# Optimization experiments

Measured on AMD Instinct MI355X. Metric: run time of the kernel, lower is better.

The kernel has to match this reference:

```python
import jax, jax.numpy as jnp
import numpy as np

N = 50000
E = 1600000
D_IN = 512   # embedding_num - 1
D_OUT = 512  # output1_dim


def setup_inputs() -> dict:
    key = jax.random.key(0)
    ks = jax.random.split(key, 16)
    A1_tensor = jax.random.normal(ks[0], (N, D_IN + 1), dtype=jnp.float32)
    adj_rows = jax.random.randint(ks[1], (E,), 0, N, dtype=jnp.int32)
    adj_cols = jax.random.randint(ks[2], (E,), 0, N, dtype=jnp.int32)
    adj_vals = jax.random.uniform(ks[3], (E,), dtype=jnp.float32)
    s = 1.0 / np.sqrt(D_IN)
    Lin1 = jax.random.uniform(ks[4], (D_IN, D_OUT), minval=-s, maxval=s, dtype=jnp.float32)
    Lin1_bias = jax.random.uniform(ks[5], (D_OUT,), minval=-s, maxval=s, dtype=jnp.float32)
    n = jax.random.uniform(ks[6], (N, 1), minval=0.0, maxval=1.0, dtype=jnp.float32)
    W1 = jax.random.uniform(ks[7], (D_IN, D_OUT), minval=-s, maxval=s, dtype=jnp.float32)
    b1 = jax.random.uniform(ks[8], (D_OUT,), minval=-s, maxval=s, dtype=jnp.float32)
    s2 = 1.0 / np.sqrt(D_OUT)
    W2 = jax.random.uniform(ks[9], (D_OUT, D_OUT), minval=-s2, maxval=s2, dtype=jnp.float32)
    b2 = jax.random.uniform(ks[10], (D_OUT,), minval=-s2, maxval=s2, dtype=jnp.float32)
    W3 = jax.random.uniform(ks[11], (D_OUT, D_OUT), minval=-s2, maxval=s2, dtype=jnp.float32)
    b3 = jax.random.uniform(ks[12], (D_OUT,), minval=-s2, maxval=s2, dtype=jnp.float32)
    return {"A1_tensor": A1_tensor, "adj_rows": adj_rows, "adj_cols": adj_cols,
            "adj_vals": adj_vals, "Lin1": Lin1, "Lin1_bias": Lin1_bias, "n": n,
            "W1": W1, "b1": b1, "W2": W2, "b2": b2, "W3": W3, "b3": b3}


def reference(A1_tensor, adj_rows, adj_cols, adj_vals, Lin1, Lin1_bias, n,
              W1, b1, W2, b2, W3, b3):
    num_nodes = A1_tensor.shape[0]

    def spmm(h):  # sparse adj @ h via edge-list gather + segment_sum
        return jax.ops.segment_sum(adj_vals[:, None] * h[adj_cols], adj_rows,
                                   num_segments=num_nodes)

    x = A1_tensor[:, 1:]                      # drop first feature column (dropout = identity at eval)
    a0 = x @ Lin1 + Lin1_bias                 # [N, D_OUT]
    a1 = a0 * n
    x1 = spmm(x @ W1 + b1)                    # gc1
    x1 = a1 + x1 * (1.0 - n)                  # gated blend
    x2 = spmm(x1 @ W2 + b2)                   # gc2
    x2 = spmm(x2 @ W3 + b3)                   # gc3
    return jnp.concatenate([x2, a0], axis=-1) # [N, 2*D_OUT]
```

## Files before the change

### kernel.cpp

```cpp
#include <hip/hip_runtime.h>
#include <stdint.h>

#define DD 512

typedef __bf16 bf16x8 __attribute__((ext_vector_type(8)));
typedef float f32x4 __attribute__((ext_vector_type(4)));

__device__ __forceinline__ unsigned short f2bf(float f) {
  uint32_t u = __builtin_bit_cast(uint32_t, f);
  u += 0x7fff + ((u >> 16) & 1);
  return (unsigned short)(u >> 16);
}
__device__ __forceinline__ float bfbits2f(uint32_t lo16) {
  return __builtin_bit_cast(float, lo16 << 16);
}

__global__ void hist_kernel(const int* __restrict__ rows, int* __restrict__ counts, int E) {
  int i = blockIdx.x * blockDim.x + threadIdx.x;
  if (i < E) atomicAdd(&counts[rows[i]], 1);
}

__global__ __launch_bounds__(256) void scan_block(const int* __restrict__ counts,
                                                  int* __restrict__ offs, int* __restrict__ bsum,
                                                  int n) {
  __shared__ int sm[256];
  int t = threadIdx.x;
  int i = blockIdx.x * 256 + t;
  int v = (i < n) ? counts[i] : 0;
  sm[t] = v;
  __syncthreads();
  for (int o = 1; o < 256; o <<= 1) {
    int x = (t >= o) ? sm[t - o] : 0;
    __syncthreads();
    sm[t] += x;
    __syncthreads();
  }
  if (i < n) offs[i + 1] = sm[t];
  if (t == 255) bsum[blockIdx.x] = sm[255];
}

__global__ __launch_bounds__(256) void scan_tops(int* __restrict__ bsum, int nb) {
  __shared__ int sm[256];
  int t = threadIdx.x;
  int v = (t < nb) ? bsum[t] : 0;
  sm[t] = v;
  __syncthreads();
  for (int o = 1; o < 256; o <<= 1) {
    int x = (t >= o) ? sm[t - o] : 0;
    __syncthreads();
    sm[t] += x;
    __syncthreads();
  }
  if (t < nb) bsum[t] = sm[t];
}

__global__ __launch_bounds__(256) void scan_add(int* __restrict__ offs,
                                                const int* __restrict__ bsum, int n) {
  int i = blockIdx.x * 256 + threadIdx.x;
  int add = (blockIdx.x > 0) ? bsum[blockIdx.x - 1] : 0;
  if (i < n) offs[i + 1] += add;
  if (i == 0) offs[0] = 0;
}

__global__ void scatter_kernel(const int* __restrict__ rows, const int* __restrict__ colsIn,
                               const float* __restrict__ valsIn, const int* __restrict__ offs,
                               int* __restrict__ cursor, int* __restrict__ colsC,
                               unsigned short* __restrict__ valsC, int E) {
  int i = blockIdx.x * blockDim.x + threadIdx.x;
  if (i < E) {
    int r = rows[i];
    int p = offs[r] + atomicAdd(&cursor[r], 1);
    colsC[p] = colsIn[i];
    valsC[p] = f2bf(valsIn[i]);
  }
}

__global__ __launch_bounds__(256) void convert_x(const float* __restrict__ A1,
                                                 __bf16* __restrict__ Xb, int N) {
  int id = blockIdx.x * 256 + threadIdx.x;
  int total = (N * DD) >> 3;
  if (id >= total) return;
  int r = id >> 6;
  int c = (id & 63) * 8;
  const float* p = A1 + (size_t)r * 513 + 1 + c;
  unsigned short h[8];
#pragma unroll
  for (int k = 0; k < 8; ++k) h[k] = f2bf(p[k]);
  uint4 o;
  o.x = (uint32_t)h[0] | ((uint32_t)h[1] << 16);
  o.y = (uint32_t)h[2] | ((uint32_t)h[3] << 16);
  o.z = (uint32_t)h[4] | ((uint32_t)h[5] << 16);
  o.w = (uint32_t)h[6] | ((uint32_t)h[7] << 16);
  *(uint4*)(Xb + (size_t)r * DD + c) = o;
}

__global__ __launch_bounds__(256) void convert_wt(const float* __restrict__ W,
                                                  __bf16* __restrict__ Wt) {
  __shared__ float tile[32][33];
  int bx = blockIdx.x * 32;
  int by = blockIdx.y * 32;
  int tx = threadIdx.x & 31, ty = threadIdx.x >> 5;
#pragma unroll
  for (int q = 0; q < 4; ++q)
    tile[ty + q * 8][tx] = W[(size_t)(by + ty + q * 8) * DD + bx + tx];
  __syncthreads();
  unsigned short* Wts = (unsigned short*)Wt;
#pragma unroll
  for (int q = 0; q < 4; ++q)
    Wts[(size_t)(bx + ty + q * 8) * DD + by + tx] = f2bf(tile[tx][ty + q * 8]);
}

template <int MODE>
__global__ __launch_bounds__(256) void gemm_mfma(
    const __bf16* __restrict__ A,
    const __bf16* __restrict__ Bt,
    const float* __restrict__ bias,
    __bf16* __restrict__ Yb,
    float* __restrict__ out,
    const float* __restrict__ nvec,
    int M) {
  __shared__ __bf16 As[128][64];
  __shared__ __bf16 Bs[128][64];
  const int tid = threadIdx.x;
  const int bx = blockIdx.x >> 2;
  const int by = blockIdx.x & 3;
  const int bm = bx * 128;
  const int bn = by * 128;
  const int lane = tid & 63;
  const int w = tid >> 6;
  const int wm = (w & 1) * 64;
  const int wn = (w >> 1) * 64;
  const int m16 = lane & 15;
  const int quad = lane >> 4;

  f32x4 acc[4][4];
#pragma unroll
  for (int i = 0; i < 4; ++i)
#pragma unroll
    for (int j = 0; j < 4; ++j) acc[i][j] = (f32x4){0.f, 0.f, 0.f, 0.f};

  const int soff = tid * 16;
  const int srow_base = soff >> 7;
  const int skb = soff & 127;

  for (int k0 = 0; k0 < DD; k0 += 64) {
#pragma unroll
    for (int q = 0; q < 4; ++q) {
      int row = q * 32 + srow_base;
      int gm = bm + row;
      if (gm >= M) gm = M - 1;
      const char* ga = (const char*)A + ((size_t)gm * DD + k0) * 2 + skb;
      char* la = (char*)&As[0][0] + q * 4096 + w * 1024;
      __builtin_amdgcn_global_load_lds(
          (const __attribute__((address_space(1))) void*)ga,
          (__attribute__((address_space(3))) void*)la, 16, 0, 0);
      const char* gb = (const char*)Bt + ((size_t)(bn + row) * DD + k0) * 2 + skb;
      char* lb = (char*)&Bs[0][0] + q * 4096 + w * 1024;
      __builtin_amdgcn_global_load_lds(
          (const __attribute__((address_space(1))) void*)gb,
          (__attribute__((address_space(3))) void*)lb, 16, 0, 0);
    }
    __syncthreads();
#pragma unroll
    for (int ks = 0; ks < 2; ++ks) {
      int kb = ks * 32 + quad * 8;
      bf16x8 af[4], bf[4];
#pragma unroll
      for (int i = 0; i < 4; ++i) af[i] = *(const bf16x8*)&As[wm + i * 16 + m16][kb];
#pragma unroll
      for (int j = 0; j < 4; ++j) bf[j] = *(const bf16x8*)&Bs[wn + j * 16 + m16][kb];
#pragma unroll
      for (int i = 0; i < 4; ++i)
#pragma unroll
        for (int j = 0; j < 4; ++j)
          acc[i][j] = __builtin_amdgcn_mfma_f32_16x16x32_bf16(af[i], bf[j], acc[i][j], 0, 0, 0);
    }
    __syncthreads();
  }

  float bv[4];
#pragma unroll
  for (int j = 0; j < 4; ++j) bv[j] = bias[bn + wn + j * 16 + m16];

  unsigned short* Ybs = (unsigned short*)Yb;
#pragma unroll
  for (int i = 0; i < 4; ++i) {
#pragma unroll
    for (int r = 0; r < 4; ++r) {
      int row = bm + wm + i * 16 + quad * 4 + r;
      if (row < M) {
        if (MODE == 0) {
          float nv = nvec[row];
#pragma unroll
          for (int j = 0; j < 4; ++j) {
            int c = bn + wn + j * 16 + m16;
            float a0 = acc[i][j][r] + bv[j];
            out[(size_t)row * 1024 + 512 + c] = a0;
            out[(size_t)row * 1024 + c] = a0 * nv;
          }
        } else {
#pragma unroll
          for (int j = 0; j < 4; ++j) {
            int c = bn + wn + j * 16 + m16;
            Ybs[(size_t)row * DD + c] = f2bf(acc[i][j][r] + bv[j]);
          }
        }
      }
    }
  }
}

template <int MODE>
__global__ __launch_bounds__(256) void spmm_bf16(
    const int* __restrict__ offs, const int* __restrict__ cols,
    const unsigned short* __restrict__ vals,
    const __bf16* __restrict__ H,
    __bf16* __restrict__ Xb, float* __restrict__ outF,
    const float* __restrict__ a1, const float* __restrict__ nvec) {
  int r = blockIdx.x;
  int t = threadIdx.x;
  int s = offs[r], e = offs[r + 1];
  int d = t * 2;
  float acc0 = 0.f, acc1 = 0.f;
  int i = s;
  for (; i + 4 <= e; i += 4) {
    int c0 = cols[i], c1 = cols[i + 1], c2 = cols[i + 2], c3 = cols[i + 3];
    float v0 = bfbits2f(vals[i]);
    float v1 = bfbits2f(vals[i + 1]);
    float v2 = bfbits2f(vals[i + 2]);
    float v3 = bfbits2f(vals[i + 3]);
    uint32_t h0 = *(const uint32_t*)(H + (size_t)c0 * DD + d);
    uint32_t h1 = *(const uint32_t*)(H + (size_t)c1 * DD + d);
    uint32_t h2 = *(const uint32_t*)(H + (size_t)c2 * DD + d);
    uint32_t h3 = *(const uint32_t*)(H + (size_t)c3 * DD + d);
    acc0 += v0 * bfbits2f(h0 & 0xffffu) + v1 * bfbits2f(h1 & 0xffffu) +
            v2 * bfbits2f(h2 & 0xffffu) + v3 * bfbits2f(h3 & 0xffffu);
    acc1 += v0 * bfbits2f(h0 >> 16) + v1 * bfbits2f(h1 >> 16) +
            v2 * bfbits2f(h2 >> 16) + v3 * bfbits2f(h3 >> 16);
  }
  for (; i < e; ++i) {
    int c = cols[i];
    float v = bfbits2f(vals[i]);
    uint32_t h = *(const uint32_t*)(H + (size_t)c * DD + d);
    acc0 += v * bfbits2f(h & 0xffffu);
    acc1 += v * bfbits2f(h >> 16);
  }
  if (MODE == 2) {
    float2 o;
    o.x = acc0;
    o.y = acc1;
    *(float2*)(outF + (size_t)r * 1024 + d) = o;
  } else {
    if (MODE == 1) {
      float g = 1.f - nvec[r];
      float2 a = *(const float2*)(a1 + (size_t)r * 1024 + d);
      acc0 = a.x + acc0 * g;
      acc1 = a.y + acc1 * g;
    }
    uint32_t p = ((uint32_t)f2bf(acc1) << 16) | (uint32_t)f2bf(acc0);
    *(uint32_t*)((unsigned short*)Xb + (size_t)r * DD + d) = p;
  }
}

extern "C" void kernel_launch(void* const* d_in, const int* in_sizes, int n_in,
                              void* d_out, int out_size, void* d_ws, size_t ws_size,
                              hipStream_t stream) {
  const float* A1       = (const float*)d_in[0];
  const int*   adj_rows = (const int*)d_in[1];
  const int*   adj_cols = (const int*)d_in[2];
  const float* adj_vals = (const float*)d_in[3];
  const float* Lin1     = (const float*)d_in[4];
  const float* Lin1b    = (const float*)d_in[5];
  const float* nvec     = (const float*)d_in[6];
  const float* W1       = (const float*)d_in[7];
  const float* b1       = (const float*)d_in[8];
  const float* W2       = (const float*)d_in[9];
  const float* b2       = (const float*)d_in[10];
  const float* W3       = (const float*)d_in[11];
  const float* b3       = (const float*)d_in[12];
  const int N = in_sizes[6];
  const int E = in_sizes[1];
  float* out = (float*)d_out;

  uint8_t* base = (uint8_t*)d_ws;
  size_t off = 0;
  auto take = [&](size_t bytes) -> void* {
    off = (off + 255) & ~(size_t)255;
    void* r = base + off;
    off += bytes;
    return r;
  };
  __bf16* Xb     = (__bf16*)take((size_t)N * DD * 2);
  __bf16* Yb     = (__bf16*)take((size_t)N * DD * 2);
  __bf16* Wt     = (__bf16*)take((size_t)4 * DD * DD * 2);
  int*    colsC  = (int*)take((size_t)E * sizeof(int));
  unsigned short* valsC = (unsigned short*)take((size_t)E * 2);
  int*    offs   = (int*)take((size_t)(N + 1) * sizeof(int));
  int*    counts = (int*)take((size_t)N * sizeof(int));
  int*    bsum   = (int*)take(1024);
  (void)ws_size; (void)n_in; (void)out_size;

  __bf16* Wt0 = Wt;
  __bf16* Wt1 = Wt + (size_t)DD * DD;
  __bf16* Wt2 = Wt + (size_t)2 * DD * DD;
  __bf16* Wt3 = Wt + (size_t)3 * DD * DD;

  int eb = (E + 255) / 256;
  int nb = (N + 255) / 256;

  hipMemsetAsync(counts, 0, (size_t)N * sizeof(int), stream);
  hist_kernel<<<eb, 256, 0, stream>>>(adj_rows, counts, E);
  scan_block<<<nb, 256, 0, stream>>>(counts, offs, bsum, N);
  scan_tops<<<1, 256, 0, stream>>>(bsum, nb);
  scan_add<<<nb, 256, 0, stream>>>(offs, bsum, N);
  hipMemsetAsync(counts, 0, (size_t)N * sizeof(int), stream);
  scatter_kernel<<<eb, 256, 0, stream>>>(adj_rows, adj_cols, adj_vals, offs, counts,
                                         colsC, valsC, E);

  convert_x<<<(N * DD / 8 + 255) / 256, 256, 0, stream>>>(A1, Xb, N);
  dim3 wgrid(16, 16);
  convert_wt<<<wgrid, 256, 0, stream>>>(Lin1, Wt0);
  convert_wt<<<wgrid, 256, 0, stream>>>(W1, Wt1);
  convert_wt<<<wgrid, 256, 0, stream>>>(W2, Wt2);
  convert_wt<<<wgrid, 256, 0, stream>>>(W3, Wt3);

  int ggrid = ((N + 127) / 128) * 4;
  gemm_mfma<0><<<ggrid, 256, 0, stream>>>(Xb, Wt0, Lin1b, nullptr, out, nvec, N);
  gemm_mfma<1><<<ggrid, 256, 0, stream>>>(Xb, Wt1, b1, Yb, nullptr, nullptr, N);
  spmm_bf16<1><<<N, 256, 0, stream>>>(offs, colsC, valsC, Yb, Xb, nullptr, out, nvec);
  gemm_mfma<1><<<ggrid, 256, 0, stream>>>(Xb, Wt2, b2, Yb, nullptr, nullptr, N);
  spmm_bf16<0><<<N, 256, 0, stream>>>(offs, colsC, valsC, Yb, Xb, nullptr, nullptr, nullptr);
  gemm_mfma<1><<<ggrid, 256, 0, stream>>>(Xb, Wt3, b3, Yb, nullptr, nullptr, N);
  spmm_bf16<2><<<N, 256, 0, stream>>>(offs, colsC, valsC, Yb, nullptr, out, nullptr, nullptr);
}
```

Measured before the change: 1.369 ms.

## Pad CSR rows to multiples of eight and vectorize SpMM gathers

Row counts are rounded up to multiples of eight in the scan, and the padded column and value arrays are zero-filled so padding slots contribute nothing (column 0, weight 0). The SpMM kernel now handles two rows per 256-thread block with 128 threads per row and four features per thread. It reads eight edges at a time with int4/uint4 loads and has no remainder loop. This cuts per-edge index and value load instructions and uses wider feature gathers. The cost is extra memset traffic, wasted work on padding edges (about 3.5 extra per row on average with ~32 edges per row), and reliance on aligned vector loads from the padded arrays.

```diff
diff --git a/kernel.cpp b/kernel.cpp
--- a/kernel.cpp
+++ b/kernel.cpp
@@ -26,7 +26,7 @@
   __shared__ int sm[256];
   int t = threadIdx.x;
   int i = blockIdx.x * 256 + t;
-  int v = (i < n) ? counts[i] : 0;
+  int v = (i < n) ? ((counts[i] + 7) & ~7) : 0;
   sm[t] = v;
   __syncthreads();
   for (int o = 1; o < 256; o <<= 1) {
@@ -216,49 +216,64 @@
     const unsigned short* __restrict__ vals,
     const __bf16* __restrict__ H,
     __bf16* __restrict__ Xb, float* __restrict__ outF,
-    const float* __restrict__ a1, const float* __restrict__ nvec) {
-  int r = blockIdx.x;
-  int t = threadIdx.x;
+    const float* __restrict__ a1, const float* __restrict__ nvec, int N) {
+  int rg = threadIdx.x >> 7;
+  int t = threadIdx.x & 127;
+  int r = blockIdx.x * 2 + rg;
+  if (r >= N) return;
+  int d = t * 4;
+  const unsigned short* Hp = (const unsigned short*)H + d;
   int s = offs[r], e = offs[r + 1];
-  int d = t * 2;
-  float acc0 = 0.f, acc1 = 0.f;
-  int i = s;
-  for (; i + 4 <= e; i += 4) {
-    int c0 = cols[i], c1 = cols[i + 1], c2 = cols[i + 2], c3 = cols[i + 3];
-    float v0 = bfbits2f(vals[i]);
-    float v1 = bfbits2f(vals[i + 1]);
-    float v2 = bfbits2f(vals[i + 2]);
-    float v3 = bfbits2f(vals[i + 3]);
-    uint32_t h0 = *(const uint32_t*)(H + (size_t)c0 * DD + d);
-    uint32_t h1 = *(const uint32_t*)(H + (size_t)c1 * DD + d);
-    uint32_t h2 = *(const uint32_t*)(H + (size_t)c2 * DD + d);
-    uint32_t h3 = *(const uint32_t*)(H + (size_t)c3 * DD + d);
-    acc0 += v0 * bfbits2f(h0 & 0xffffu) + v1 * bfbits2f(h1 & 0xffffu) +
-            v2 * bfbits2f(h2 & 0xffffu) + v3 * bfbits2f(h3 & 0xffffu);
-    acc1 += v0 * bfbits2f(h0 >> 16) + v1 * bfbits2f(h1 >> 16) +
-            v2 * bfbits2f(h2 >> 16) + v3 * bfbits2f(h3 >> 16);
-  }
-  for (; i < e; ++i) {
-    int c = cols[i];
-    float v = bfbits2f(vals[i]);
-    uint32_t h = *(const uint32_t*)(H + (size_t)c * DD + d);
-    acc0 += v * bfbits2f(h & 0xffffu);
-    acc1 += v * bfbits2f(h >> 16);
-  }
+
+  float ac0 = 0.f, ac1 = 0.f, ac2 = 0.f, ac3 = 0.f;
+  for (int i = s; i < e; i += 8) {
+    int4 ca = *(const int4*)(cols + i);
+    int4 cb = *(const int4*)(cols + i + 4);
+    uint4 vw = *(const uint4*)(vals + i);
+    uint2 h[8];
+    h[0] = *(const uint2*)(Hp + (size_t)ca.x * DD);
+    h[1] = *(const uint2*)(Hp + (size_t)ca.y * DD);
+    h[2] = *(const uint2*)(Hp + (size_t)ca.z * DD);
+    h[3] = *(const uint2*)(Hp + (size_t)ca.w * DD);
+    h[4] = *(const uint2*)(Hp + (size_t)cb.x * DD);
+    h[5] = *(const uint2*)(Hp + (size_t)cb.y * DD);
+    h[6] = *(const uint2*)(Hp + (size_t)cb.z * DD);
+    h[7] = *(const uint2*)(Hp + (size_t)cb.w * DD);
+    float v[8];
+    v[0] = bfbits2f(vw.x & 0xffffu);
+    v[1] = bfbits2f(vw.x >> 16);
+    v[2] = bfbits2f(vw.y & 0xffffu);
+    v[3] = bfbits2f(vw.y >> 16);
+    v[4] = bfbits2f(vw.z & 0xffffu);
+    v[5] = bfbits2f(vw.z >> 16);
+    v[6] = bfbits2f(vw.w & 0xffffu);
+    v[7] = bfbits2f(vw.w >> 16);
+#pragma unroll
+    for (int k = 0; k < 8; ++k) {
+      ac0 += v[k] * bfbits2f(h[k].x & 0xffffu);
+      ac1 += v[k] * bfbits2f(h[k].x >> 16);
+      ac2 += v[k] * bfbits2f(h[k].y & 0xffffu);
+      ac3 += v[k] * bfbits2f(h[k].y >> 16);
+    }
+  }
+
   if (MODE == 2) {
-    float2 o;
-    o.x = acc0;
-    o.y = acc1;
-    *(float2*)(outF + (size_t)r * 1024 + d) = o;
+    float4 o;
+    o.x = ac0; o.y = ac1; o.z = ac2; o.w = ac3;
+    *(float4*)(outF + (size_t)r * 1024 + d) = o;
   } else {
     if (MODE == 1) {
       float g = 1.f - nvec[r];
-      float2 a = *(const float2*)(a1 + (size_t)r * 1024 + d);
-      acc0 = a.x + acc0 * g;
-      acc1 = a.y + acc1 * g;
-    }
-    uint32_t p = ((uint32_t)f2bf(acc1) << 16) | (uint32_t)f2bf(acc0);
-    *(uint32_t*)((unsigned short*)Xb + (size_t)r * DD + d) = p;
+      float4 a = *(const float4*)(a1 + (size_t)r * 1024 + d);
+      ac0 = a.x + ac0 * g;
+      ac1 = a.y + ac1 * g;
+      ac2 = a.z + ac2 * g;
+      ac3 = a.w + ac3 * g;
+    }
+    uint2 p;
+    p.x = ((uint32_t)f2bf(ac1) << 16) | (uint32_t)f2bf(ac0);
+    p.y = ((uint32_t)f2bf(ac3) << 16) | (uint32_t)f2bf(ac2);
+    *(uint2*)((unsigned short*)Xb + (size_t)r * DD + d) = p;
   }
 }
 
@@ -290,11 +305,12 @@
     off += bytes;
     return r;
   };
+  const size_t EP = (size_t)E + 8 * (size_t)N;
   __bf16* Xb     = (__bf16*)take((size_t)N * DD * 2);
   __bf16* Yb     = (__bf16*)take((size_t)N * DD * 2);
   __bf16* Wt     = (__bf16*)take((size_t)4 * DD * DD * 2);
-  int*    colsC  = (int*)take((size_t)E * sizeof(int));
-  unsigned short* valsC = (unsigned short*)take((size_t)E * 2);
+  int*    colsC  = (int*)take(EP * sizeof(int));
+  unsigned short* valsC = (unsigned short*)take(EP * 2);
   int*    offs   = (int*)take((size_t)(N + 1) * sizeof(int));
   int*    counts = (int*)take((size_t)N * sizeof(int));
   int*    bsum   = (int*)take(1024);
@@ -309,6 +325,8 @@
   int nb = (N + 255) / 256;
 
   hipMemsetAsync(counts, 0, (size_t)N * sizeof(int), stream);
+  hipMemsetAsync(colsC, 0, EP * sizeof(int), stream);
+  hipMemsetAsync(valsC, 0, EP * 2, stream);
   hist_kernel<<<eb, 256, 0, stream>>>(adj_rows, counts, E);
   scan_block<<<nb, 256, 0, stream>>>(counts, offs, bsum, N);
   scan_tops<<<1, 256, 0, stream>>>(bsum, nb);
@@ -325,11 +343,13 @@
   convert_wt<<<wgrid, 256, 0, stream>>>(W3, Wt3);
 
   int ggrid = ((N + 127) / 128) * 4;
+  int sgrid = (N + 1) / 2;
+
   gemm_mfma<0><<<ggrid, 256, 0, stream>>>(Xb, Wt0, Lin1b, nullptr, out, nvec, N);
   gemm_mfma<1><<<ggrid, 256, 0, stream>>>(Xb, Wt1, b1, Yb, nullptr, nullptr, N);
-  spmm_bf16<1><<<N, 256, 0, stream>>>(offs, colsC, valsC, Yb, Xb, nullptr, out, nvec);
+  spmm_bf16<1><<<sgrid, 256, 0, stream>>>(offs, colsC, valsC, Yb, Xb, nullptr, out, nvec, N);
   gemm_mfma<1><<<ggrid, 256, 0, stream>>>(Xb, Wt2, b2, Yb, nullptr, nullptr, N);
-  spmm_bf16<0><<<N, 256, 0, stream>>>(offs, colsC, valsC, Yb, Xb, nullptr, nullptr, nullptr);
+  spmm_bf16<0><<<sgrid, 256, 0, stream>>>(offs, colsC, valsC, Yb, Xb, nullptr, nullptr, nullptr, N);
   gemm_mfma<1><<<ggrid, 256, 0, stream>>>(Xb, Wt3, b3, Yb, nullptr, nullptr, N);
-  spmm_bf16<2><<<N, 256, 0, stream>>>(offs, colsC, valsC, Yb, nullptr, out, nullptr, nullptr);
-}
+  spmm_bf16<2><<<sgrid, 256, 0, stream>>>(offs, colsC, valsC, Yb, nullptr, out, nullptr, nullptr, N);
+}
```

Measured after the change: 1.381 ms. About the same (+0.9%).
